# Optimization experiments

Measured on AMD Instinct MI355X. Metric: run time of the kernel, lower is better.

The kernel has to match this reference:

```python
import jax, jax.numpy as jnp
import numpy as np


def _box_iou(a, b):
    # a: [K,4], b: [K,4] in ltrb; returns [K,K] pairwise IoU (torchvision box_iou math)
    area_a = jnp.clip(a[:, 2] - a[:, 0], 0) * jnp.clip(a[:, 3] - a[:, 1], 0)
    area_b = jnp.clip(b[:, 2] - b[:, 0], 0) * jnp.clip(b[:, 3] - b[:, 1], 0)
    lt = jnp.maximum(a[:, None, :2], b[None, :, :2])
    rb = jnp.minimum(a[:, None, 2:], b[None, :, 2:])
    wh = jnp.clip(rb - lt, 0)
    inter = wh[..., 0] * wh[..., 1]
    return inter / (area_a[:, None] + area_b[None, :] - inter + 1e-9)


def _nms_class(score, boxes, th_c, nms_th, K):
    # score: [N], boxes: [N,4]. Keep boxes with score > th_c, take top-K by score,
    # then greedy NMS suppressing lower-scored boxes with IoU >= nms_th (original keeps iou < nms_th).
    masked = jnp.where(score > th_c, score, -jnp.inf)
    top_s, idx = jax.lax.top_k(masked, K)          # descending score order
    valid = top_s > -jnp.inf
    bk = boxes[idx]                                 # [K,4]
    iou = _box_iou(bk, bk)                          # [K,K]
    order = jnp.arange(K)

    def body(alive, i):
        keep_i = alive[i]
        suppress = keep_i & (iou[i] >= nms_th) & (order > i)
        return alive & ~suppress, keep_i

    _, keep = jax.lax.scan(body, valid, order)
    return jnp.where(keep[:, None], bk, 0.0), jnp.where(keep, top_s, 0.0), keep


def decode(bboxes_in, scores_in, dboxes_xywh, conf_th, nms_th, max_num, scale_xy, scale_wh):
    B, C = bboxes_in.shape[0], scores_in.shape[1]
    K = int(max_num)
    # scale_back_batch: xywh offsets -> ltrb absolute boxes, softmax over classes
    b = jnp.transpose(bboxes_in, (0, 2, 1))                         # [B,N,4]
    xy = scale_xy * b[..., :2] * dboxes_xywh[..., 2:] + dboxes_xywh[..., :2]
    wh = jnp.exp(scale_wh * b[..., 2:]) * dboxes_xywh[..., 2:]
    ltrb = jnp.concatenate([xy - 0.5 * wh, xy + 0.5 * wh], axis=-1)  # [B,N,4]
    probs = jax.nn.softmax(jnp.transpose(scores_in, (0, 2, 1)), axis=-1)  # [B,N,C]
    cls_scores = jnp.transpose(probs[..., 1:], (0, 2, 1))            # [B,C-1,N] (skip background cls 0)

    def per_image(scores_cn, boxes_n4):
        f = jax.vmap(lambda s, t: _nms_class(s, boxes_n4, t, nms_th, K))
        return f(scores_cn, conf_th)

    bk, sk, keep = jax.vmap(per_image)(cls_scores, ltrb)  # [B,C-1,K,4], [B,C-1,K], [B,C-1,K]
    M = (C - 1) * K
    labels = jnp.arange(1, C, dtype=jnp.float32)[None, :, None] * keep.astype(jnp.float32)
    return (bk.reshape(B, M, 4), labels.reshape(B, M), sk.reshape(B, M), keep.reshape(B, M))


def setup_inputs() -> dict:
    key = jax.random.key(0)
    k0, k1, k2, k3, k4 = jax.random.split(key, 5)
    B, N, C = 32, 24564, 21
    bboxes_in = 0.5 * jax.random.normal(k0, (B, 4, N), jnp.float32)
    scores_in = jax.random.normal(k1, (B, C, N), jnp.float32)
    cxy = jax.random.uniform(k2, (1, N, 2), jnp.float32)
    dwh = jax.random.uniform(k3, (1, N, 2), jnp.float32, 0.05, 0.5)
    dboxes_xywh = jnp.concatenate([cxy, dwh], axis=-1)
    conf_th = jax.random.uniform(k4, (C - 1,), jnp.float32, 0.01, 0.05)
    return {
        'bboxes_in': bboxes_in,
        'scores_in': scores_in,
        'dboxes_xywh': dboxes_xywh,
        'conf_th': conf_th,
        'nms_th': jnp.float32(0.5),
        'max_num': 200,
        'scale_xy': 0.1,
        'scale_wh': 0.2,
    }


def reference(bboxes_in, scores_in, dboxes_xywh, conf_th, nms_th, max_num, scale_xy, scale_wh):
    # Padded, jit-compatible equivalent of the torch Decoder: per image we return
    # [(C-1)*K] slots of (boxes, labels, scores) with a boolean keep-mask; the torch
    # version returns only the kept (variable-length) entries, in the same order.
    return decode(bboxes_in, scores_in, dboxes_xywh, conf_th, nms_th, max_num, scale_xy, scale_wh)
```

## Files before the change

kernel.cpp:

```cpp
#include <hip/hip_runtime.h>
#include <math.h>

typedef unsigned int uint;
typedef unsigned short u16;
typedef unsigned long long u64;

#define NT 256
#define KTOP 200
#define CAP 256
#define CAPC 3072
#define SEGS 4
#define SEGCAP 512
#define NCLS 21
#define C1 20
#define MROWS 208
#define NSPLIT 48

__device__ __forceinline__ u64 flip64(double d) {
  u64 u = (u64)__double_as_longlong(d);
  return (u & 0x8000000000000000ULL) ? ~u : (u | 0x8000000000000000ULL);
}

__device__ __forceinline__ double unflip64(u64 k) {
  u64 u = (k & 0x8000000000000000ULL) ? (k ^ 0x8000000000000000ULL) : ~k;
  return __longlong_as_double((long long)u);
}

__device__ __forceinline__ uint q_key16(float sf) {
  float qf = (sf + 16.0f) * 4096.0f;
  qf = fmaxf(fminf(qf, 65535.0f), 1.0f);
  return (uint)qf;
}

__device__ __forceinline__ void par_walk(const uint* hist, uint* scan, u64* wm,
                                         uint* res, uint rank, int tid) {
  scan[tid] = hist[tid];
  __syncthreads();
#pragma unroll
  for (int off = 1; off < 256; off <<= 1) {
    uint v = scan[tid];
    uint a = (tid + off < 256) ? scan[tid + off] : 0u;
    __syncthreads();
    scan[tid] = v + a;
    __syncthreads();
  }
  u64 m = __ballot(scan[tid] >= rank);
  if ((tid & 63) == 0) wm[tid >> 6] = m;
  __syncthreads();
  if (tid == 0) {
    int bin = 0;
    for (int w = 3; w >= 0; --w) {
      if (wm[w]) { bin = w * 64 + (63 - __clzll(wm[w])); break; }
    }
    res[0] = (uint)bin;
    res[1] = scan[bin];
    res[2] = hist[bin];
  }
  __syncthreads();
}

__global__ __launch_bounds__(NT) void prep_kernel(
    const float* __restrict__ bboxes, const float* __restrict__ scores,
    const float* __restrict__ dboxes, const float* __restrict__ conf_th,
    const float* __restrict__ scale_xy_p, const float* __restrict__ scale_wh_p,
    float4* __restrict__ boxes_out, double* __restrict__ lse_out,
    u16* __restrict__ keys_out, uint* __restrict__ ghist,
    int B, int N, int npad, int perblk)
{
  __shared__ double s_logth[C1];
  __shared__ uint lhist[C1 * 256];
  int tid = threadIdx.x;
  if (tid < C1) s_logth[tid] = log((double)conf_th[tid]);
  for (int i = tid; i < C1 * 256; i += NT) lhist[i] = 0;
  __syncthreads();

  int b = blockIdx.x / NSPLIT, j = blockIdx.x - b * NSPLIT;
  int s0 = j * perblk, e0 = min(N, s0 + perblk);
  float sxy = *scale_xy_p, swh = *scale_wh_p;

  for (int n = s0 + tid; n < e0; n += NT) {
    int gid = b * N + n;
    const float* bb = bboxes + (size_t)b * 4 * N + n;
    float bx = bb[0];
    float by = bb[(size_t)N];
    float bw = bb[2 * (size_t)N];
    float bh = bb[3 * (size_t)N];
    float4 d = reinterpret_cast<const float4*>(dboxes)[n];
    float x = sxy * bx * d.z + d.x;
    float y = sxy * by * d.w + d.y;
    float w = expf(swh * bw) * d.z;
    float h = expf(swh * bh) * d.w;
    boxes_out[gid] = make_float4(x - 0.5f * w, y - 0.5f * h, x + 0.5f * w, y + 0.5f * h);

    const float* sc = scores + (size_t)b * NCLS * N + n;
    float v[NCLS];
    float mx = -INFINITY;
#pragma unroll
    for (int c = 0; c < NCLS; ++c) { v[c] = sc[(size_t)c * N]; mx = fmaxf(mx, v[c]); }
    double sum0 = 0.0, sum1 = 0.0, sum2 = 0.0;
#pragma unroll
    for (int c = 0; c < NCLS; ++c) {
      float e = __expf(v[c] - mx);
      if ((c % 3) == 0) sum0 += (double)e;
      else if ((c % 3) == 1) sum1 += (double)e;
      else sum2 += (double)e;
    }
    double lse = (double)mx + log(sum0 + sum1 + sum2);
    lse_out[gid] = lse;

#pragma unroll
    for (int c = 0; c < C1; ++c) {
      double s = (double)v[c + 1] - lse;
      uint key = 0;
      if (s > s_logth[c]) key = q_key16((float)s);
      keys_out[((size_t)b * C1 + c) * npad + n] = (u16)key;
      if (key) atomicAdd(&lhist[c * 256 + (key >> 8)], 1u);
    }
  }
  if (j == NSPLIT - 1 && npad > N) {
    int pad = npad - N;
    for (int t = tid; t < pad * C1; t += NT) {
      int c = t / pad, n = N + (t - c * pad);
      keys_out[((size_t)b * C1 + c) * npad + n] = 0;
    }
  }
  __syncthreads();
  for (int i = tid; i < C1 * 256; i += NT) {
    uint v = lhist[i];
    if (v) atomicAdd(&ghist[((size_t)b * C1 + (i >> 8)) * 256 + (i & 255)], v);
  }
}

__global__ __launch_bounds__(NT) void collect_kernel(
    const u16* __restrict__ keys, const uint* __restrict__ ghist,
    uint4* __restrict__ L0cnt, uint* __restrict__ cand, uint* __restrict__ cnts,
    int npad)
{
  int blk = blockIdx.x;
  int task = blk >> 2, seg = blk & (SEGS - 1);
  int tid = threadIdx.x, lane = tid & 63;
  __shared__ uint sL, sCnt0, sCnt;

  if (tid < 64) {
    uint4 h = reinterpret_cast<const uint4*>(ghist + (size_t)task * 256)[tid];
    uint s = h.x + h.y + h.z + h.w;
    uint suf = s;
#pragma unroll
    for (int off = 1; off < 64; off <<= 1) {
      uint o = (uint)__shfl_down((int)suf, off);
      if (lane + off < 64) suf += o;
    }
    uint total = (uint)__shfl((int)suf, 0);
    uint sn = (uint)__shfl_down((int)suf, 1);
    if (lane == 63) sn = 0;
    uint c3 = h.w + sn, c2 = c3 + h.z, c1 = c2 + h.y, c0 = c1 + h.x;
    uint binoff, cnt, abv;
    if (c3 >= KTOP)      { binoff = 3; cnt = c3; abv = c3 - h.w; }
    else if (c2 >= KTOP) { binoff = 2; cnt = c2; abv = c2 - h.z; }
    else if (c1 >= KTOP) { binoff = 1; cnt = c1; abv = c1 - h.y; }
    else                 { binoff = 0; cnt = c0; abv = c0 - h.x; }
    uint L0v, cnt0v, abovev;
    if (total < KTOP) {
      L0v = 1u; cnt0v = total; abovev = 0u;
    } else {
      u64 m = __ballot(suf >= KTOP);
      int l = 63 - __clzll(m);
      uint bo = (uint)__shfl((int)binoff, l);
      cnt0v = (uint)__shfl((int)cnt, l);
      abovev = (uint)__shfl((int)abv, l);
      L0v = ((uint)(4 * l) + bo) << 8;
    }
    if (lane == 0) {
      sL = L0v; sCnt0 = cnt0v;
      if (seg == 0) L0cnt[task] = make_uint4(L0v, cnt0v, abovev, total);
    }
  }
  if (tid == NT - 1) sCnt = 0;
  __syncthreads();

  uint L = sL, cnt0 = sCnt0;
  if (cnt0 > CAPC) { if (tid == 0) cnts[blk] = 0; return; }

  const u16* krow = keys + (size_t)task * npad;
  const uint4* krow8 = reinterpret_cast<const uint4*>(krow);
  int nv8 = npad >> 3;
  int per8 = (nv8 + SEGS - 1) >> 2;
  int s8 = seg * per8, e8 = min(nv8, s8 + per8);
  uint* myc = cand + ((size_t)task * SEGS + seg) * SEGCAP;

  for (int i = s8 + tid; i < e8; i += NT) {
    uint4 kv = krow8[i];
    uint base = (uint)(i << 3);
    uint ks[8] = { kv.x & 0xFFFFu, kv.x >> 16, kv.y & 0xFFFFu, kv.y >> 16,
                   kv.z & 0xFFFFu, kv.z >> 16, kv.w & 0xFFFFu, kv.w >> 16 };
#pragma unroll
    for (int comp = 0; comp < 8; ++comp) {
      uint k = ks[comp];
      bool f = (k >= L);
      u64 m = __ballot(f);
      if (m) {
        uint nb = (uint)__popcll(m);
        uint wb = 0;
        if (lane == 0) wb = atomicAdd(&sCnt, nb);
        wb = (uint)__shfl((int)wb, 0);
        if (f) {
          uint pos = wb + (uint)__popcll(m & ((1ULL << lane) - 1ULL));
          if (pos < SEGCAP) myc[pos] = (k << 15) | (base + comp);
        }
      }
    }
  }
  __syncthreads();
  if (tid == 0) cnts[blk] = sCnt;
}

__global__ __launch_bounds__(NT) void topk_kernel(
    const u16* __restrict__ keys, const uint4* __restrict__ L0cnt,
    const uint* __restrict__ candg, const uint* __restrict__ cnts,
    const float* __restrict__ scores, const double* __restrict__ lse,
    const float4* __restrict__ boxesws,
    u64* __restrict__ tkeys, float4* __restrict__ tbox, uint* __restrict__ tcnt,
    int B, int N, int npad)
{
  int task = blockIdx.x;
  int b = task / C1, c = task - b * C1;
  int tid = threadIdx.x, lane = tid & 63;
  const u16* krow = keys + (size_t)task * npad;
  int nv8 = npad >> 3;

  __shared__ uint cand[CAPC];
  __shared__ uint histB[256];
  __shared__ uint scanB[256];
  __shared__ u64 wmB[4];
  __shared__ uint res3[4];
  __shared__ uint scq[SEGS];
  __shared__ int si[CAP];
  __shared__ u64 sC[CAP];
  __shared__ float4 sbx[CAP];
  __shared__ uint sCnt, sCnt2;

  uint4 w0 = L0cnt[task];
  uint cnt0 = w0.y;
  if (tid < SEGS) scq[tid] = cnts[task * SEGS + tid];
  if (tid == 0) { sCnt = 0; sCnt2 = 0; }
  __syncthreads();
  bool slow = (cnt0 > CAPC) ||
              (scq[0] > SEGCAP) || (scq[1] > SEGCAP) ||
              (scq[2] > SEGCAP) || (scq[3] > SEGCAP);

  uint pref = w0.x >> 8, above = w0.z, rank = KTOP - w0.z;
  uint cnt;

  if (!slow) {
    uint off1 = scq[0], off2 = off1 + scq[1], off3 = off2 + scq[2];
    cnt = off3 + scq[3];
    const uint* cg = candg + (size_t)task * SEGS * SEGCAP;
    for (int j = tid; j < (int)scq[0]; j += NT) cand[j] = cg[j];
    for (int j = tid; j < (int)scq[1]; j += NT) cand[off1 + j] = cg[SEGCAP + j];
    for (int j = tid; j < (int)scq[2]; j += NT) cand[off2 + j] = cg[2 * SEGCAP + j];
    for (int j = tid; j < (int)scq[3]; j += NT) cand[off3 + j] = cg[3 * SEGCAP + j];
    __syncthreads();
  } else {
    const uint4* krow8 = reinterpret_cast<const uint4*>(krow);
    histB[tid] = 0;
    __syncthreads();
    for (int i = tid; i < nv8; i += NT) {
      uint4 kv = krow8[i];
      uint ks[8] = { kv.x & 0xFFFFu, kv.x >> 16, kv.y & 0xFFFFu, kv.y >> 16,
                     kv.z & 0xFFFFu, kv.z >> 16, kv.w & 0xFFFFu, kv.w >> 16 };
#pragma unroll
      for (int comp = 0; comp < 8; ++comp) {
        uint k = ks[comp];
        if ((k >> 8) == pref) atomicAdd(&histB[k & 255u], 1u);
      }
    }
    __syncthreads();
    par_walk(histB, scanB, wmB, res3, rank, tid);
    uint Ts = (pref << 8) | res3[0];
    for (int i = tid; i < nv8; i += NT) {
      uint4 kv = krow8[i];
      uint base = (uint)(i << 3);
      uint ks[8] = { kv.x & 0xFFFFu, kv.x >> 16, kv.y & 0xFFFFu, kv.y >> 16,
                     kv.z & 0xFFFFu, kv.z >> 16, kv.w & 0xFFFFu, kv.w >> 16 };
#pragma unroll
      for (int comp = 0; comp < 8; ++comp) {
        uint k = ks[comp];
        bool f = (k >= Ts);
        u64 m = __ballot(f);
        if (m) {
          uint nb = (uint)__popcll(m);
          uint wb = 0;
          if (lane == 0) wb = atomicAdd(&sCnt, nb);
          wb = (uint)__shfl((int)wb, 0);
          if (f) {
            uint pos = wb + (uint)__popcll(m & ((1ULL << lane) - 1ULL));
            if (pos < CAPC) cand[pos] = (k << 15) | (base + comp);
          }
        }
      }
    }
    __syncthreads();
    cnt = min(sCnt, (uint)CAPC);
  }

  uint cntF;
  if (cnt <= CAP) {
    for (int p = tid; p < (int)cnt; p += NT) si[p] = (int)(cand[p] & 0x7FFFu);
    __syncthreads();
    cntF = cnt;
  } else {
    histB[tid] = 0;
    __syncthreads();
    for (int p = tid; p < (int)cnt; p += NT) {
      uint k = cand[p] >> 15;
      if ((k >> 8) == pref) atomicAdd(&histB[k & 255u], 1u);
    }
    __syncthreads();
    par_walk(histB, scanB, wmB, res3, rank, tid);
    uint T = (pref << 8) | res3[0];
    for (int p = tid; p < (int)cnt; p += NT) {
      uint cd = cand[p];
      if ((cd >> 15) >= T) {
        uint q = atomicAdd(&sCnt2, 1u);
        if (q < CAP) si[q] = (int)(cd & 0x7FFFu);
      }
    }
    __syncthreads();
    cntF = min(sCnt2, (uint)CAP);
  }

  {
    int p = tid;
    u64 C;
    if (p < (int)cntF) {
      int n = si[p];
      double s = (double)scores[((size_t)b * NCLS + (c + 1)) * N + n] - lse[(size_t)b * N + n];
      u64 f = flip64(s);
      C = (f & ~0x7FFFULL) | (u64)(32767 - n);
      sbx[p] = boxesws[(size_t)b * N + n];
    } else {
      C = (u64)p;
      sbx[p] = make_float4(0.f, 0.f, 0.f, 0.f);
    }
    sC[p] = C;
  }
  __syncthreads();

  {
    u64 kp = sC[tid];
    int r = 0;
#pragma unroll 8
    for (int jj = 0; jj < CAP; ++jj) r += (sC[jj] > kp) ? 1 : 0;
    if (r < KTOP) {
      tkeys[(size_t)task * KTOP + r] = kp;
      tbox[(size_t)task * KTOP + r] = sbx[tid];
    }
  }
  if (tid == 0) tcnt[task] = min(cntF, (uint)KTOP);
}

__global__ __launch_bounds__(NT) void maskresolve_kernel(
    const u64* __restrict__ tkeys, const float4* __restrict__ tbox,
    const uint* __restrict__ tcnt, const float* __restrict__ nms_th_p,
    float* __restrict__ out, int B)
{
  int task = blockIdx.x;
  int b = task / C1, c = task - b * C1;
  int tid = threadIdx.x, lane = tid & 63, wav = tid >> 6;

  __shared__ float4 sbox[MROWS];
  __shared__ float sar[MROWS];
  __shared__ u64 smaskT[13][64];
  __shared__ u64 saliveW[4];

  int valid = (int)tcnt[task];
  float nth = *nms_th_p;

  if (tid < MROWS) {
    float4 bx = (tid < valid) ? tbox[(size_t)task * KTOP + tid]
                              : make_float4(0.f, 0.f, 0.f, 0.f);
    sbox[tid] = bx;
    sar[tid] = fmaxf(bx.z - bx.x, 0.f) * fmaxf(bx.w - bx.y, 0.f);
  }
  __syncthreads();

  {
    float4 jb0 = sbox[lane], jb1 = sbox[lane + 64], jb2 = sbox[lane + 128];
    float4 jb3 = (lane + 192 < MROWS) ? sbox[lane + 192]
                                      : make_float4(0.f, 0.f, 0.f, 0.f);
    float ja0 = sar[lane], ja1 = sar[lane + 64], ja2 = sar[lane + 128],
          ja3 = (lane + 192 < MROWS) ? sar[lane + 192] : 0.f;
    for (int w = wav; w < 13; w += 4) {
      u64 word = 0;
      int r0 = w * 16;
#pragma unroll
      for (int rr = 0; rr < 16; ++rr) {
        int r = r0 + rr;
        float4 rb = sbox[r];
        float ra = sar[r];
        uint nib = 0;
#define IOU_BIT(K, JB, JA) { \
        int j = lane + 64 * (K); \
        float xx1 = fmaxf(rb.x, JB.x), yy1 = fmaxf(rb.y, JB.y); \
        float xx2 = fminf(rb.z, JB.z), yy2 = fminf(rb.w, JB.w); \
        float ww = fmaxf(xx2 - xx1, 0.f), hh = fmaxf(yy2 - yy1, 0.f); \
        float inter = ww * hh; \
        float den = ((ra + JA) - inter) + 1e-9f; \
        if ((inter >= nth * den) && (j > r)) nib |= 1u << (K); }
        IOU_BIT(0, jb0, ja0) IOU_BIT(1, jb1, ja1)
        IOU_BIT(2, jb2, ja2) IOU_BIT(3, jb3, ja3)
#undef IOU_BIT
        word |= (u64)nib << (rr * 4);
      }
      smaskT[w][lane] = word;
    }
  }
  __syncthreads();

  if (tid < 64) {
    u64 mm[13];
#pragma unroll
    for (int w = 0; w < 13; ++w) mm[w] = smaskT[w][lane];
    uint av = 0;
#pragma unroll
    for (int k = 0; k < 4; ++k)
      if (lane + 64 * k < valid) av |= 1u << k;
#define STEP(i) { \
    u64 bm = __ballot((lane == ((i) & 63)) && ((av >> ((i) >> 6)) & 1u)); \
    if (bm) av &= ~((uint)((mm[(i) >> 4] >> (((i) & 15) * 4)) & 0xFULL)); }
#define S4(i)  STEP(i) STEP((i)+1) STEP((i)+2) STEP((i)+3)
#define S16(i) S4(i) S4((i)+4) S4((i)+8) S4((i)+12)
#define S64(i) S16(i) S16((i)+16) S16((i)+32) S16((i)+48)
    S64(0) S64(64) S64(128) S16(192)
#undef S64
#undef S16
#undef S4
#undef STEP
#pragma unroll
    for (int k = 0; k < 4; ++k) {
      u64 bb = __ballot((av >> k) & 1u);
      if (lane == 0) saliveW[k] = bb;
    }
  }
  __syncthreads();

  size_t M = (size_t)C1 * KTOP;
  float* out_boxes  = out;
  float* out_labels = out + (size_t)B * M * 4;
  float* out_scores = out_labels + (size_t)B * M;
  float* out_keep   = out_scores + (size_t)B * M;
  if (tid < KTOP) {
    size_t slot = ((size_t)b * C1 + c) * KTOP + tid;
    bool kept = (tid < valid) && ((saliveW[tid >> 6] >> (tid & 63)) & 1ULL);
    float4 bx = kept ? sbox[tid] : make_float4(0.f, 0.f, 0.f, 0.f);
    reinterpret_cast<float4*>(out_boxes)[slot] = bx;
    out_labels[slot] = kept ? (float)(c + 1) : 0.0f;
    out_scores[slot] = kept ? (float)exp(unflip64(tkeys[(size_t)task * KTOP + tid])) : 0.0f;
    out_keep[slot]   = kept ? 1.0f : 0.0f;
  }
}

extern "C" void kernel_launch(void* const* d_in, const int* in_sizes, int n_in,
                              void* d_out, int out_size, void* d_ws, size_t ws_size,
                              hipStream_t stream) {
  const float* bboxes   = (const float*)d_in[0];
  const float* scores   = (const float*)d_in[1];
  const float* dboxes   = (const float*)d_in[2];
  const float* conf_th  = (const float*)d_in[3];
  const float* nms_th   = (const float*)d_in[4];
  const float* scale_xy = (const float*)d_in[6];
  const float* scale_wh = (const float*)d_in[7];

  int N = in_sizes[2] / 4;
  int B = in_sizes[0] / (4 * N);
  int npad = (N + 7) & ~7;

  char* ws = (char*)d_ws;
  size_t off = 0;
  double* lse     = (double*)(ws + off); off += (size_t)B * N * 8;
  float4* boxesws = (float4*)(ws + off); off += (size_t)B * N * 16;
  u16*    keys    = (u16*)   (ws + off); off += (size_t)B * C1 * npad * 2;
  uint*   ghist   = (uint*)  (ws + off); off += (size_t)B * C1 * 256 * 4;
  uint4*  L0cnt   = (uint4*) (ws + off); off += (size_t)B * C1 * 16;
  uint*   cand    = (uint*)  (ws + off); off += (size_t)B * C1 * SEGS * SEGCAP * 4;
  uint*   cnts    = (uint*)  (ws + off); off += (size_t)B * C1 * SEGS * 4;
  u64*    tkeys   = (u64*)   (ws + off); off += (size_t)B * C1 * KTOP * 8;
  float4* tbox    = (float4*)(ws + off); off += (size_t)B * C1 * KTOP * 16;
  uint*   tcnt    = (uint*)  (ws + off);

  hipMemsetAsync(ghist, 0, (size_t)B * C1 * 256 * 4, stream);

  int perblk = (N + NSPLIT - 1) / NSPLIT;
  prep_kernel<<<B * NSPLIT, NT, 0, stream>>>(
      bboxes, scores, dboxes, conf_th, scale_xy, scale_wh,
      boxesws, lse, keys, ghist, B, N, npad, perblk);

  collect_kernel<<<B * C1 * SEGS, NT, 0, stream>>>(
      keys, ghist, L0cnt, cand, cnts, npad);

  topk_kernel<<<B * C1, NT, 0, stream>>>(
      keys, L0cnt, cand, cnts, scores, lse, boxesws, tkeys, tbox, tcnt, B, N, npad);

  maskresolve_kernel<<<B * C1, NT, 0, stream>>>(
      tkeys, tbox, tcnt, nms_th, (float*)d_out, B);
}
```

Measured before the change: 94.64 us.

## Decode boxes lazily in topk and replace global histogram atomics with per-block slices

Box decoding moves out of prep_kernel into topk_kernel, so only the selected top-K candidates are decoded instead of writing all B*N boxes to workspace and reading them back. Each prep block now writes its local histogram to its own global slice instead of issuing atomics into a shared histogram. That also removes the memset, and a new walk_kernel reduces the slices and computes the per-task threshold once instead of in every collect block. The cost is an extra kernel launch, a larger histogram workspace (NSPLIT times bigger) that walk_kernel must read, and scattered bbox reads inside topk.

```diff
diff --git a/kernel.cpp b/kernel.cpp
--- a/kernel.cpp
+++ b/kernel.cpp
@@ -60,11 +60,9 @@
 }
 
 __global__ __launch_bounds__(NT) void prep_kernel(
-    const float* __restrict__ bboxes, const float* __restrict__ scores,
-    const float* __restrict__ dboxes, const float* __restrict__ conf_th,
-    const float* __restrict__ scale_xy_p, const float* __restrict__ scale_wh_p,
-    float4* __restrict__ boxes_out, double* __restrict__ lse_out,
-    u16* __restrict__ keys_out, uint* __restrict__ ghist,
+    const float* __restrict__ scores, const float* __restrict__ conf_th,
+    double* __restrict__ lse_out, u16* __restrict__ keys_out,
+    uint* __restrict__ ghist,
     int B, int N, int npad, int perblk)
 {
   __shared__ double s_logth[C1];
@@ -76,22 +74,9 @@
 
   int b = blockIdx.x / NSPLIT, j = blockIdx.x - b * NSPLIT;
   int s0 = j * perblk, e0 = min(N, s0 + perblk);
-  float sxy = *scale_xy_p, swh = *scale_wh_p;
 
   for (int n = s0 + tid; n < e0; n += NT) {
     int gid = b * N + n;
-    const float* bb = bboxes + (size_t)b * 4 * N + n;
-    float bx = bb[0];
-    float by = bb[(size_t)N];
-    float bw = bb[2 * (size_t)N];
-    float bh = bb[3 * (size_t)N];
-    float4 d = reinterpret_cast<const float4*>(dboxes)[n];
-    float x = sxy * bx * d.z + d.x;
-    float y = sxy * by * d.w + d.y;
-    float w = expf(swh * bw) * d.z;
-    float h = expf(swh * bh) * d.w;
-    boxes_out[gid] = make_float4(x - 0.5f * w, y - 0.5f * h, x + 0.5f * w, y + 0.5f * h);
-
     const float* sc = scores + (size_t)b * NCLS * N + n;
     float v[NCLS];
     float mx = -INFINITY;
@@ -125,60 +110,66 @@
     }
   }
   __syncthreads();
-  for (int i = tid; i < C1 * 256; i += NT) {
-    uint v = lhist[i];
-    if (v) atomicAdd(&ghist[((size_t)b * C1 + (i >> 8)) * 256 + (i & 255)], v);
-  }
+  uint* gslice = ghist + (size_t)(b * NSPLIT + j) * C1 * 256;
+  for (int i = tid; i < C1 * 256; i += NT) gslice[i] = lhist[i];
+}
+
+__global__ __launch_bounds__(64) void walk_kernel(
+    const uint* __restrict__ ghist, uint4* __restrict__ L0cnt, int B)
+{
+  int task = blockIdx.x;
+  int b = task / C1, c = task - b * C1;
+  int lane = threadIdx.x;
+  uint4 h = make_uint4(0, 0, 0, 0);
+  for (int j = 0; j < NSPLIT; ++j) {
+    const uint4* sl = reinterpret_cast<const uint4*>(
+        ghist + ((size_t)(b * NSPLIT + j) * C1 + c) * 256);
+    uint4 t = sl[lane];
+    h.x += t.x; h.y += t.y; h.z += t.z; h.w += t.w;
+  }
+  uint s = h.x + h.y + h.z + h.w;
+  uint suf = s;
+#pragma unroll
+  for (int off = 1; off < 64; off <<= 1) {
+    uint o = (uint)__shfl_down((int)suf, off);
+    if (lane + off < 64) suf += o;
+  }
+  uint total = (uint)__shfl((int)suf, 0);
+  uint sn = (uint)__shfl_down((int)suf, 1);
+  if (lane == 63) sn = 0;
+  uint c3 = h.w + sn, c2 = c3 + h.z, c1 = c2 + h.y, c0 = c1 + h.x;
+  uint binoff, cnt, abv;
+  if (c3 >= KTOP)      { binoff = 3; cnt = c3; abv = c3 - h.w; }
+  else if (c2 >= KTOP) { binoff = 2; cnt = c2; abv = c2 - h.z; }
+  else if (c1 >= KTOP) { binoff = 1; cnt = c1; abv = c1 - h.y; }
+  else                 { binoff = 0; cnt = c0; abv = c0 - h.x; }
+  uint L0v, cnt0v, abovev;
+  if (total < KTOP) {
+    L0v = 1u; cnt0v = total; abovev = 0u;
+  } else {
+    u64 m = __ballot(suf >= KTOP);
+    int l = 63 - __clzll(m);
+    uint bo = (uint)__shfl((int)binoff, l);
+    cnt0v = (uint)__shfl((int)cnt, l);
+    abovev = (uint)__shfl((int)abv, l);
+    L0v = ((uint)(4 * l) + bo) << 8;
+  }
+  if (lane == 0) L0cnt[task] = make_uint4(L0v, cnt0v, abovev, total);
 }
 
 __global__ __launch_bounds__(NT) void collect_kernel(
-    const u16* __restrict__ keys, const uint* __restrict__ ghist,
-    uint4* __restrict__ L0cnt, uint* __restrict__ cand, uint* __restrict__ cnts,
-    int npad)
+    const u16* __restrict__ keys, const uint4* __restrict__ L0cnt,
+    uint* __restrict__ cand, uint* __restrict__ cnts, int npad)
 {
   int blk = blockIdx.x;
   int task = blk >> 2, seg = blk & (SEGS - 1);
   int tid = threadIdx.x, lane = tid & 63;
-  __shared__ uint sL, sCnt0, sCnt;
-
-  if (tid < 64) {
-    uint4 h = reinterpret_cast<const uint4*>(ghist + (size_t)task * 256)[tid];
-    uint s = h.x + h.y + h.z + h.w;
-    uint suf = s;
-#pragma unroll
-    for (int off = 1; off < 64; off <<= 1) {
-      uint o = (uint)__shfl_down((int)suf, off);
-      if (lane + off < 64) suf += o;
-    }
-    uint total = (uint)__shfl((int)suf, 0);
-    uint sn = (uint)__shfl_down((int)suf, 1);
-    if (lane == 63) sn = 0;
-    uint c3 = h.w + sn, c2 = c3 + h.z, c1 = c2 + h.y, c0 = c1 + h.x;
-    uint binoff, cnt, abv;
-    if (c3 >= KTOP)      { binoff = 3; cnt = c3; abv = c3 - h.w; }
-    else if (c2 >= KTOP) { binoff = 2; cnt = c2; abv = c2 - h.z; }
-    else if (c1 >= KTOP) { binoff = 1; cnt = c1; abv = c1 - h.y; }
-    else                 { binoff = 0; cnt = c0; abv = c0 - h.x; }
-    uint L0v, cnt0v, abovev;
-    if (total < KTOP) {
-      L0v = 1u; cnt0v = total; abovev = 0u;
-    } else {
-      u64 m = __ballot(suf >= KTOP);
-      int l = 63 - __clzll(m);
-      uint bo = (uint)__shfl((int)binoff, l);
-      cnt0v = (uint)__shfl((int)cnt, l);
-      abovev = (uint)__shfl((int)abv, l);
-      L0v = ((uint)(4 * l) + bo) << 8;
-    }
-    if (lane == 0) {
-      sL = L0v; sCnt0 = cnt0v;
-      if (seg == 0) L0cnt[task] = make_uint4(L0v, cnt0v, abovev, total);
-    }
-  }
-  if (tid == NT - 1) sCnt = 0;
-  __syncthreads();
-
-  uint L = sL, cnt0 = sCnt0;
+  __shared__ uint sCnt;
+  if (tid == 0) sCnt = 0;
+  __syncthreads();
+
+  uint4 w0 = L0cnt[task];
+  uint L = w0.x, cnt0 = w0.y;
   if (cnt0 > CAPC) { if (tid == 0) cnts[blk] = 0; return; }
 
   const u16* krow = keys + (size_t)task * npad;
@@ -218,7 +209,8 @@
     const u16* __restrict__ keys, const uint4* __restrict__ L0cnt,
     const uint* __restrict__ candg, const uint* __restrict__ cnts,
     const float* __restrict__ scores, const double* __restrict__ lse,
-    const float4* __restrict__ boxesws,
+    const float* __restrict__ bboxes, const float* __restrict__ dboxes,
+    const float* __restrict__ scale_xy_p, const float* __restrict__ scale_wh_p,
     u64* __restrict__ tkeys, float4* __restrict__ tbox, uint* __restrict__ tcnt,
     int B, int N, int npad)
 {
@@ -330,6 +322,7 @@
   }
 
   {
+    float sxy = *scale_xy_p, swh = *scale_wh_p;
     int p = tid;
     u64 C;
     if (p < (int)cntF) {
@@ -337,7 +330,17 @@
       double s = (double)scores[((size_t)b * NCLS + (c + 1)) * N + n] - lse[(size_t)b * N + n];
       u64 f = flip64(s);
       C = (f & ~0x7FFFULL) | (u64)(32767 - n);
-      sbx[p] = boxesws[(size_t)b * N + n];
+      const float* bb = bboxes + (size_t)b * 4 * N + n;
+      float bx = bb[0];
+      float by = bb[(size_t)N];
+      float bw = bb[2 * (size_t)N];
+      float bh = bb[3 * (size_t)N];
+      float4 d = reinterpret_cast<const float4*>(dboxes)[n];
+      float x = sxy * bx * d.z + d.x;
+      float y = sxy * by * d.w + d.y;
+      float w = expf(swh * bw) * d.z;
+      float h = expf(swh * bh) * d.w;
+      sbx[p] = make_float4(x - 0.5f * w, y - 0.5f * h, x + 0.5f * w, y + 0.5f * h);
     } else {
       C = (u64)p;
       sbx[p] = make_float4(0.f, 0.f, 0.f, 0.f);
@@ -478,9 +481,8 @@
   char* ws = (char*)d_ws;
   size_t off = 0;
   double* lse     = (double*)(ws + off); off += (size_t)B * N * 8;
-  float4* boxesws = (float4*)(ws + off); off += (size_t)B * N * 16;
   u16*    keys    = (u16*)   (ws + off); off += (size_t)B * C1 * npad * 2;
-  uint*   ghist   = (uint*)  (ws + off); off += (size_t)B * C1 * 256 * 4;
+  uint*   ghist   = (uint*)  (ws + off); off += (size_t)B * NSPLIT * C1 * 256 * 4;
   uint4*  L0cnt   = (uint4*) (ws + off); off += (size_t)B * C1 * 16;
   uint*   cand    = (uint*)  (ws + off); off += (size_t)B * C1 * SEGS * SEGCAP * 4;
   uint*   cnts    = (uint*)  (ws + off); off += (size_t)B * C1 * SEGS * 4;
@@ -488,18 +490,18 @@
   float4* tbox    = (float4*)(ws + off); off += (size_t)B * C1 * KTOP * 16;
   uint*   tcnt    = (uint*)  (ws + off);
 
-  hipMemsetAsync(ghist, 0, (size_t)B * C1 * 256 * 4, stream);
-
   int perblk = (N + NSPLIT - 1) / NSPLIT;
   prep_kernel<<<B * NSPLIT, NT, 0, stream>>>(
-      bboxes, scores, dboxes, conf_th, scale_xy, scale_wh,
-      boxesws, lse, keys, ghist, B, N, npad, perblk);
+      scores, conf_th, lse, keys, ghist, B, N, npad, perblk);
+
+  walk_kernel<<<B * C1, 64, 0, stream>>>(ghist, L0cnt, B);
 
   collect_kernel<<<B * C1 * SEGS, NT, 0, stream>>>(
-      keys, ghist, L0cnt, cand, cnts, npad);
+      keys, L0cnt, cand, cnts, npad);
 
   topk_kernel<<<B * C1, NT, 0, stream>>>(
-      keys, L0cnt, cand, cnts, scores, lse, boxesws, tkeys, tbox, tcnt, B, N, npad);
+      keys, L0cnt, cand, cnts, scores, lse, bboxes, dboxes,
+      scale_xy, scale_wh, tkeys, tbox, tcnt, B, N, npad);
 
   maskresolve_kernel<<<B * C1, NT, 0, stream>>>(
       tkeys, tbox, tcnt, nms_th, (float*)d_out, B);
```

Result: slower. 98.08 us (+3.6%).

## Fuse top-k with NMS, decode boxes lazily, vectorize softmax over pairs

Applied to the files above, without the earlier changes.

Merges the top-k and mask-resolve kernels into one final kernel, so the sorted keys and boxes stay in shared memory and no longer go through global workspace. Box decoding moves out of the prep pass and runs only for the selected candidates, which removes the full B*N float4 write and the bbox reads from prep. Prep now handles two anchors per thread with float2 loads and packed key stores, and the memset is replaced by a small zeroing kernel. In exchange the fused kernel uses more shared memory and may run at lower occupancy, and the paired loads assume N is even.

```diff
diff --git a/kernel.cpp b/kernel.cpp
--- a/kernel.cpp
+++ b/kernel.cpp
@@ -59,12 +59,14 @@
   __syncthreads();
 }
 
+__global__ __launch_bounds__(NT) void zero_ghist(uint* __restrict__ g) {
+  g[(size_t)blockIdx.x * NT + threadIdx.x] = 0;
+}
+
 __global__ __launch_bounds__(NT) void prep_kernel(
-    const float* __restrict__ bboxes, const float* __restrict__ scores,
-    const float* __restrict__ dboxes, const float* __restrict__ conf_th,
-    const float* __restrict__ scale_xy_p, const float* __restrict__ scale_wh_p,
-    float4* __restrict__ boxes_out, double* __restrict__ lse_out,
-    u16* __restrict__ keys_out, uint* __restrict__ ghist,
+    const float* __restrict__ scores, const float* __restrict__ conf_th,
+    double* __restrict__ lse_out, u16* __restrict__ keys_out,
+    uint* __restrict__ ghist,
     int B, int N, int npad, int perblk)
 {
   __shared__ double s_logth[C1];
@@ -76,45 +78,46 @@
 
   int b = blockIdx.x / NSPLIT, j = blockIdx.x - b * NSPLIT;
   int s0 = j * perblk, e0 = min(N, s0 + perblk);
-  float sxy = *scale_xy_p, swh = *scale_wh_p;
-
-  for (int n = s0 + tid; n < e0; n += NT) {
-    int gid = b * N + n;
-    const float* bb = bboxes + (size_t)b * 4 * N + n;
-    float bx = bb[0];
-    float by = bb[(size_t)N];
-    float bw = bb[2 * (size_t)N];
-    float bh = bb[3 * (size_t)N];
-    float4 d = reinterpret_cast<const float4*>(dboxes)[n];
-    float x = sxy * bx * d.z + d.x;
-    float y = sxy * by * d.w + d.y;
-    float w = expf(swh * bw) * d.z;
-    float h = expf(swh * bh) * d.w;
-    boxes_out[gid] = make_float4(x - 0.5f * w, y - 0.5f * h, x + 0.5f * w, y + 0.5f * h);
-
+  int half = (e0 - s0) >> 1;
+
+  for (int p = tid; p < half; p += NT) {
+    int n = s0 + 2 * p;
     const float* sc = scores + (size_t)b * NCLS * N + n;
-    float v[NCLS];
-    float mx = -INFINITY;
-#pragma unroll
-    for (int c = 0; c < NCLS; ++c) { v[c] = sc[(size_t)c * N]; mx = fmaxf(mx, v[c]); }
-    double sum0 = 0.0, sum1 = 0.0, sum2 = 0.0;
+    float2 v[NCLS];
+    float mx0 = -INFINITY, mx1 = -INFINITY;
 #pragma unroll
     for (int c = 0; c < NCLS; ++c) {
-      float e = __expf(v[c] - mx);
-      if ((c % 3) == 0) sum0 += (double)e;
-      else if ((c % 3) == 1) sum1 += (double)e;
-      else sum2 += (double)e;
-    }
-    double lse = (double)mx + log(sum0 + sum1 + sum2);
-    lse_out[gid] = lse;
+      float2 t = *reinterpret_cast<const float2*>(sc + (size_t)c * N);
+      v[c] = t;
+      mx0 = fmaxf(mx0, t.x);
+      mx1 = fmaxf(mx1, t.y);
+    }
+    double a0 = 0.0, a1 = 0.0, a2 = 0.0;
+    double b0 = 0.0, b1 = 0.0, b2 = 0.0;
+#pragma unroll
+    for (int c = 0; c < NCLS; ++c) {
+      float e0f = __expf(v[c].x - mx0);
+      float e1f = __expf(v[c].y - mx1);
+      if ((c % 3) == 0)      { a0 += (double)e0f; b0 += (double)e1f; }
+      else if ((c % 3) == 1) { a1 += (double)e0f; b1 += (double)e1f; }
+      else                   { a2 += (double)e0f; b2 += (double)e1f; }
+    }
+    double lse0 = (double)mx0 + log(a0 + a1 + a2);
+    double lse1 = (double)mx1 + log(b0 + b1 + b2);
+    double2 lw; lw.x = lse0; lw.y = lse1;
+    reinterpret_cast<double2*>(lse_out + (size_t)b * N + n)[0] = lw;
 
 #pragma unroll
     for (int c = 0; c < C1; ++c) {
-      double s = (double)v[c + 1] - lse;
-      uint key = 0;
-      if (s > s_logth[c]) key = q_key16((float)s);
-      keys_out[((size_t)b * C1 + c) * npad + n] = (u16)key;
-      if (key) atomicAdd(&lhist[c * 256 + (key >> 8)], 1u);
+      double s0d = (double)v[c + 1].x - lse0;
+      double s1d = (double)v[c + 1].y - lse1;
+      uint k0 = 0, k1 = 0;
+      if (s0d > s_logth[c]) k0 = q_key16((float)s0d);
+      if (s1d > s_logth[c]) k1 = q_key16((float)s1d);
+      *reinterpret_cast<uint*>(keys_out + ((size_t)b * C1 + c) * npad + n)
+          = k0 | (k1 << 16);
+      if (k0) atomicAdd(&lhist[c * 256 + (k0 >> 8)], 1u);
+      if (k1) atomicAdd(&lhist[c * 256 + (k1 >> 8)], 1u);
     }
   }
   if (j == NSPLIT - 1 && npad > N) {
@@ -126,8 +129,8 @@
   }
   __syncthreads();
   for (int i = tid; i < C1 * 256; i += NT) {
-    uint v = lhist[i];
-    if (v) atomicAdd(&ghist[((size_t)b * C1 + (i >> 8)) * 256 + (i & 255)], v);
+    uint v2 = lhist[i];
+    if (v2) atomicAdd(&ghist[((size_t)b * C1 + (i >> 8)) * 256 + (i & 255)], v2);
   }
 }
 
@@ -214,17 +217,18 @@
   if (tid == 0) cnts[blk] = sCnt;
 }
 
-__global__ __launch_bounds__(NT) void topk_kernel(
+__global__ __launch_bounds__(NT) void final_kernel(
     const u16* __restrict__ keys, const uint4* __restrict__ L0cnt,
     const uint* __restrict__ candg, const uint* __restrict__ cnts,
     const float* __restrict__ scores, const double* __restrict__ lse,
-    const float4* __restrict__ boxesws,
-    u64* __restrict__ tkeys, float4* __restrict__ tbox, uint* __restrict__ tcnt,
-    int B, int N, int npad)
+    const float* __restrict__ bboxes, const float* __restrict__ dboxes,
+    const float* __restrict__ scale_xy_p, const float* __restrict__ scale_wh_p,
+    const float* __restrict__ nms_th_p,
+    float* __restrict__ out, int B, int N, int npad)
 {
   int task = blockIdx.x;
   int b = task / C1, c = task - b * C1;
-  int tid = threadIdx.x, lane = tid & 63;
+  int tid = threadIdx.x, lane = tid & 63, wav = tid >> 6;
   const u16* krow = keys + (size_t)task * npad;
   int nv8 = npad >> 3;
 
@@ -236,13 +240,19 @@
   __shared__ uint scq[SEGS];
   __shared__ int si[CAP];
   __shared__ u64 sC[CAP];
+  __shared__ u64 skid[CAP];
   __shared__ float4 sbx[CAP];
+  __shared__ float4 sbox[MROWS];
+  __shared__ float sar[MROWS];
+  __shared__ u64 smaskT[13][64];
+  __shared__ u64 saliveW[4];
   __shared__ uint sCnt, sCnt2;
 
   uint4 w0 = L0cnt[task];
   uint cnt0 = w0.y;
   if (tid < SEGS) scq[tid] = cnts[task * SEGS + tid];
   if (tid == 0) { sCnt = 0; sCnt2 = 0; }
+  if (tid < MROWS) { sbox[tid] = make_float4(0.f, 0.f, 0.f, 0.f); sar[tid] = 0.f; }
   __syncthreads();
   bool slow = (cnt0 > CAPC) ||
               (scq[0] > SEGCAP) || (scq[1] > SEGCAP) ||
@@ -329,7 +339,10 @@
     cntF = min(sCnt2, (uint)CAP);
   }
 
+  int valid_cnt = (int)min(cntF, (uint)KTOP);
+
   {
+    float sxy = *scale_xy_p, swh = *scale_wh_p;
     int p = tid;
     u64 C;
     if (p < (int)cntF) {
@@ -337,7 +350,17 @@
       double s = (double)scores[((size_t)b * NCLS + (c + 1)) * N + n] - lse[(size_t)b * N + n];
       u64 f = flip64(s);
       C = (f & ~0x7FFFULL) | (u64)(32767 - n);
-      sbx[p] = boxesws[(size_t)b * N + n];
+      const float* bb = bboxes + (size_t)b * 4 * N + n;
+      float bx = bb[0];
+      float by = bb[(size_t)N];
+      float bw = bb[2 * (size_t)N];
+      float bh = bb[3 * (size_t)N];
+      float4 d = reinterpret_cast<const float4*>(dboxes)[n];
+      float x = sxy * bx * d.z + d.x;
+      float y = sxy * by * d.w + d.y;
+      float w = expf(swh * bw) * d.z;
+      float h = expf(swh * bh) * d.w;
+      sbx[p] = make_float4(x - 0.5f * w, y - 0.5f * h, x + 0.5f * w, y + 0.5f * h);
     } else {
       C = (u64)p;
       sbx[p] = make_float4(0.f, 0.f, 0.f, 0.f);
@@ -351,38 +374,16 @@
     int r = 0;
 #pragma unroll 8
     for (int jj = 0; jj < CAP; ++jj) r += (sC[jj] > kp) ? 1 : 0;
-    if (r < KTOP) {
-      tkeys[(size_t)task * KTOP + r] = kp;
-      tbox[(size_t)task * KTOP + r] = sbx[tid];
-    }
-  }
-  if (tid == 0) tcnt[task] = min(cntF, (uint)KTOP);
-}
-
-__global__ __launch_bounds__(NT) void maskresolve_kernel(
-    const u64* __restrict__ tkeys, const float4* __restrict__ tbox,
-    const uint* __restrict__ tcnt, const float* __restrict__ nms_th_p,
-    float* __restrict__ out, int B)
-{
-  int task = blockIdx.x;
-  int b = task / C1, c = task - b * C1;
-  int tid = threadIdx.x, lane = tid & 63, wav = tid >> 6;
-
-  __shared__ float4 sbox[MROWS];
-  __shared__ float sar[MROWS];
-  __shared__ u64 smaskT[13][64];
-  __shared__ u64 saliveW[4];
-
-  int valid = (int)tcnt[task];
+    if (tid < (int)cntF && r < KTOP) {
+      skid[r] = kp;
+      float4 bx = sbx[tid];
+      sbox[r] = bx;
+      sar[r] = fmaxf(bx.z - bx.x, 0.f) * fmaxf(bx.w - bx.y, 0.f);
+    }
+  }
+  __syncthreads();
+
   float nth = *nms_th_p;
-
-  if (tid < MROWS) {
-    float4 bx = (tid < valid) ? tbox[(size_t)task * KTOP + tid]
-                              : make_float4(0.f, 0.f, 0.f, 0.f);
-    sbox[tid] = bx;
-    sar[tid] = fmaxf(bx.z - bx.x, 0.f) * fmaxf(bx.w - bx.y, 0.f);
-  }
-  __syncthreads();
 
   {
     float4 jb0 = sbox[lane], jb1 = sbox[lane + 64], jb2 = sbox[lane + 128];
@@ -424,7 +425,7 @@
     uint av = 0;
 #pragma unroll
     for (int k = 0; k < 4; ++k)
-      if (lane + 64 * k < valid) av |= 1u << k;
+      if (lane + 64 * k < valid_cnt) av |= 1u << k;
 #define STEP(i) { \
     u64 bm = __ballot((lane == ((i) & 63)) && ((av >> ((i) >> 6)) & 1u)); \
     if (bm) av &= ~((uint)((mm[(i) >> 4] >> (((i) & 15) * 4)) & 0xFULL)); }
@@ -438,8 +439,8 @@
 #undef STEP
 #pragma unroll
     for (int k = 0; k < 4; ++k) {
-      u64 bb = __ballot((av >> k) & 1u);
-      if (lane == 0) saliveW[k] = bb;
+      u64 bb2 = __ballot((av >> k) & 1u);
+      if (lane == 0) saliveW[k] = bb2;
     }
   }
   __syncthreads();
@@ -451,11 +452,11 @@
   float* out_keep   = out_scores + (size_t)B * M;
   if (tid < KTOP) {
     size_t slot = ((size_t)b * C1 + c) * KTOP + tid;
-    bool kept = (tid < valid) && ((saliveW[tid >> 6] >> (tid & 63)) & 1ULL);
+    bool kept = (tid < valid_cnt) && ((saliveW[tid >> 6] >> (tid & 63)) & 1ULL);
     float4 bx = kept ? sbox[tid] : make_float4(0.f, 0.f, 0.f, 0.f);
     reinterpret_cast<float4*>(out_boxes)[slot] = bx;
     out_labels[slot] = kept ? (float)(c + 1) : 0.0f;
-    out_scores[slot] = kept ? (float)exp(unflip64(tkeys[(size_t)task * KTOP + tid])) : 0.0f;
+    out_scores[slot] = kept ? (float)exp(unflip64(skid[tid])) : 0.0f;
     out_keep[slot]   = kept ? 1.0f : 0.0f;
   }
 }
@@ -478,29 +479,22 @@
   char* ws = (char*)d_ws;
   size_t off = 0;
   double* lse     = (double*)(ws + off); off += (size_t)B * N * 8;
-  float4* boxesws = (float4*)(ws + off); off += (size_t)B * N * 16;
   u16*    keys    = (u16*)   (ws + off); off += (size_t)B * C1 * npad * 2;
   uint*   ghist   = (uint*)  (ws + off); off += (size_t)B * C1 * 256 * 4;
   uint4*  L0cnt   = (uint4*) (ws + off); off += (size_t)B * C1 * 16;
   uint*   cand    = (uint*)  (ws + off); off += (size_t)B * C1 * SEGS * SEGCAP * 4;
-  uint*   cnts    = (uint*)  (ws + off); off += (size_t)B * C1 * SEGS * 4;
-  u64*    tkeys   = (u64*)   (ws + off); off += (size_t)B * C1 * KTOP * 8;
-  float4* tbox    = (float4*)(ws + off); off += (size_t)B * C1 * KTOP * 16;
-  uint*   tcnt    = (uint*)  (ws + off);
-
-  hipMemsetAsync(ghist, 0, (size_t)B * C1 * 256 * 4, stream);
-
-  int perblk = (N + NSPLIT - 1) / NSPLIT;
+  uint*   cnts    = (uint*)  (ws + off);
+
+  zero_ghist<<<B * C1, NT, 0, stream>>>(ghist);
+
+  int perblk = ((N + NSPLIT - 1) / NSPLIT + 1) & ~1;
   prep_kernel<<<B * NSPLIT, NT, 0, stream>>>(
-      bboxes, scores, dboxes, conf_th, scale_xy, scale_wh,
-      boxesws, lse, keys, ghist, B, N, npad, perblk);
+      scores, conf_th, lse, keys, ghist, B, N, npad, perblk);
 
   collect_kernel<<<B * C1 * SEGS, NT, 0, stream>>>(
       keys, ghist, L0cnt, cand, cnts, npad);
 
-  topk_kernel<<<B * C1, NT, 0, stream>>>(
-      keys, L0cnt, cand, cnts, scores, lse, boxesws, tkeys, tbox, tcnt, B, N, npad);
-
-  maskresolve_kernel<<<B * C1, NT, 0, stream>>>(
-      tkeys, tbox, tcnt, nms_th, (float*)d_out, B);
-}
+  final_kernel<<<B * C1, NT, 0, stream>>>(
+      keys, L0cnt, cand, cnts, scores, lse, bboxes, dboxes,
+      scale_xy, scale_wh, nms_th, (float*)d_out, B, N, npad);
+}
```

Result: no change. 93.55 us (-1.1%).
